# Kernel tuning notes

Measured on AMD Instinct MI355X. Metric: run time of the kernel, lower is better.

## Reference

```python
import jax, jax.numpy as jnp
import numpy as np

EPS = 1e-6

def _conv1x1(x, w, b):
    # x: [b,c,h,w], w: [o,c], b: [o] -> per-pixel matmul
    return jnp.einsum('bchw,oc->bohw', x, w) + b[None, :, None, None]

def setup_inputs() -> dict:
    key = jax.random.key(0)
    ks = jax.random.split(key, 10)
    b, c, h, w = 16, 256, 128, 128
    dec = jax.random.normal(ks[0], (b, c, h, w), jnp.float32)
    enc = jax.random.normal(ks[1], (b, c, h, w), jnp.float32)
    ln_w = jnp.ones((c,), jnp.float32)
    ln_b = jnp.zeros((c,), jnp.float32)
    w0 = jax.random.normal(ks[2], (c, c), jnp.float32) * 0.05
    b0 = jax.random.normal(ks[3], (c,), jnp.float32) * 0.05
    w1 = jax.random.normal(ks[4], (c // 2, c), jnp.float32) * 0.05
    b1 = jax.random.normal(ks[5], (c // 2,), jnp.float32) * 0.05
    w2 = jax.random.normal(ks[6], (c // 4, c // 2), jnp.float32) * 0.05
    b2 = jax.random.normal(ks[7], (c // 4,), jnp.float32) * 0.05
    w3 = jax.random.normal(ks[8], (1, c // 4), jnp.float32) * 0.05
    b3 = jax.random.normal(ks[9], (1,), jnp.float32) * 0.05
    return dict(dec=dec, enc=enc, ln_w=ln_w, ln_b=ln_b, w0=w0, b0=b0,
                w1=w1, b1=b1, w2=w2, b2=b2, w3=w3, b3=b3)

def reference(dec, enc, ln_w, ln_b, w0, b0, w1, b1, w2, b2, w3, b3):
    b, c, h, w = dec.shape
    x = dec + enc
    # LayerNorm2d: normalize over channel dim per pixel (biased var, eps=1e-6)
    mu = jnp.mean(x, axis=1, keepdims=True)
    var = jnp.var(x, axis=1, keepdims=True)
    x = (x - mu) / jnp.sqrt(var + EPS) * ln_w[None, :, None, None] + ln_b[None, :, None, None]
    # in_conv: 1x1 conv + exact GELU
    x = jax.nn.gelu(_conv1x1(x, w0, b0), approximate=False)
    # split: local channels kept, global channels pooled and broadcast back
    local_x = x[:, :c // 2]                                   # [b,c/2,h,w]
    global_x = jnp.mean(x[:, c // 2:], axis=(2, 3), keepdims=True)  # [b,c/2,1,1]
    x = jnp.concatenate([local_x, jnp.broadcast_to(global_x, local_x.shape)], axis=1)
    # mask_pre: nc -> nc/2 -> nc/4 -> 1 with GELUs
    x = jax.nn.gelu(_conv1x1(x, w1, b1), approximate=False)
    x = jax.nn.gelu(_conv1x1(x, w2, b2), approximate=False)
    x = _conv1x1(x, w3, b3)
    return jax.nn.sigmoid(x)
```

## Files before the change

kernel.cpp:

```cpp
#include <hip/hip_runtime.h>
#include <math.h>

typedef float f32x4 __attribute__((ext_vector_type(4)));
typedef short s8v __attribute__((ext_vector_type(8)));
typedef unsigned int u32x4 __attribute__((ext_vector_type(4)));

#define LN_EPS 1e-6f

static __device__ __forceinline__ unsigned short f2bf(float f) {
  union { float f; unsigned int u; } v; v.f = f;
  unsigned int r = (v.u + 0x7FFFu + ((v.u >> 16) & 1u)) >> 16;
  return (unsigned short)r;
}
static __device__ __forceinline__ float bf2f(unsigned short b) {
  union { float f; unsigned int u; } v; v.u = ((unsigned int)b) << 16;
  return v.f;
}
static __device__ __forceinline__ unsigned int f2bf_pk(float lo, float hi) {
  unsigned int r;
  asm("v_cvt_pk_bf16_f32 %0, %1, %2" : "=v"(r) : "v"(lo), "v"(hi));
  return r;
}
static __device__ __forceinline__ float gelu_fast(float x) {
  float t = x * x;
  float u = x * fmaf(t, 0.07135481283f, 1.5957691216f);
  float e = __expf(-u);
  return __fdividef(x, 1.0f + e);
}

__global__ void prep_kernel(const float* __restrict__ w0, const float* __restrict__ w1,
                            const float* __restrict__ w2, const float* __restrict__ lnw,
                            const float* __restrict__ lnb, const float* __restrict__ b0,
                            unsigned short* __restrict__ wt0f, unsigned short* __restrict__ w1f,
                            unsigned short* __restrict__ w2f, float* __restrict__ gacc,
                            float* __restrict__ sfold, float* __restrict__ tfold) {
  int idx = blockIdx.x * blockDim.x + threadIdx.x;
  int stride = gridDim.x * blockDim.x;
  const int N0 = 65536, N1 = 16384, N2 = 8192, N3 = 2048, N4 = 256;
  for (int i = idx; i < N0 + N1 + N2 + N3 + N4; i += stride) {
    if (i < N0) {
      int j = i & 7, l = (i >> 3) & 63, ks = (i >> 9) & 7, n0 = i >> 12;
      int k = ks * 32 + (l >> 4) * 8 + j;
      wt0f[i] = f2bf(w0[(n0 * 16 + (l & 15)) * 256 + k] * lnw[k]);
    } else if (i < N0 + N1) {
      int t = i - N0;
      int j = t & 7, l = (t >> 3) & 63, ks = (t >> 9) & 3, n0 = t >> 11;
      w1f[t] = f2bf(w1[(n0 * 16 + (l & 15)) * 256 + ks * 32 + (l >> 4) * 8 + j]);
    } else if (i < N0 + N1 + N2) {
      int t = i - N0 - N1;
      int j = t & 7, l = (t >> 3) & 63, ks = (t >> 9) & 3, n0 = t >> 11;
      w2f[t] = f2bf(w2[(n0 * 16 + (l & 15)) * 128 + ks * 32 + (l >> 4) * 8 + j]);
    } else if (i < N0 + N1 + N2 + N3) {
      gacc[i - N0 - N1 - N2] = 0.0f;
    } else {
      int n = i - N0 - N1 - N2 - N3;
      float s = 0.f, t = 0.f;
      for (int c = 0; c < 256; ++c) {
        float wv = w0[n * 256 + c];
        s += wv * lnw[c];
        t += wv * lnb[c];
      }
      sfold[n] = s;
      tfold[n] = t + b0[n];
    }
  }
}

__global__ __launch_bounds__(256, 4) void k1_kernel(
    const float* __restrict__ dec, const float* __restrict__ enc,
    const unsigned short* __restrict__ wt0f,
    const float* __restrict__ sfold, const float* __restrict__ tfold,
    unsigned short* __restrict__ yl, float* __restrict__ gacc) {
  __shared__ __align__(16) unsigned char At[64 * 512];
  __shared__ float wred[4][16][8];
  __shared__ float alphaL[64], betaL[64];

  const int tid = threadIdx.x, blk = blockIdx.x;
  const int b = blk >> 8;
  const int hw0 = (blk & 255) << 6;
  const int g = tid >> 4, kq = tid & 15;
  const int lane = tid & 63, w = tid >> 6, l15 = lane & 15, lg = lane >> 4;

  f32x4 sum = {0.f, 0.f, 0.f, 0.f}, sq = {0.f, 0.f, 0.f, 0.f};
  const long base = (long)(b * 256) * 16384 + hw0 + (kq << 2);
#pragma unroll
  for (int it = 0; it < 2; ++it) {
    f32x4 xv[8];
#pragma unroll
    for (int s = 0; s < 8; ++s) {
      const int c = it * 128 + g * 8 + s;
      f32x4 d = *(const f32x4*)(dec + base + (long)c * 16384);
      f32x4 e = *(const f32x4*)(enc + base + (long)c * 16384);
      f32x4 x = d + e;
      xv[s] = x;
      sum += x;
      sq += x * x;
    }
#pragma unroll
    for (int px = 0; px < 4; ++px) {
      const int p = (kq << 2) + px;
      u32x4 hv;
#pragma unroll
      for (int sp = 0; sp < 4; ++sp)
        hv[sp] = f2bf_pk(xv[2 * sp][px], xv[2 * sp + 1][px]);
      const int byte = (p * 512 + it * 256 + g * 16) ^ ((p & 7) << 4);
      *(u32x4*)(&At[byte]) = hv;
    }
  }

#pragma unroll
  for (int q = 0; q < 4; ++q) {
    sum[q] += __shfl_xor(sum[q], 16, 64);
    sq[q] += __shfl_xor(sq[q], 16, 64);
    sum[q] += __shfl_xor(sum[q], 32, 64);
    sq[q] += __shfl_xor(sq[q], 32, 64);
  }
  if (lane < 16) {
#pragma unroll
    for (int q = 0; q < 4; ++q) { wred[w][lane][q] = sum[q]; wred[w][lane][4 + q] = sq[q]; }
  }
  __syncthreads();
  if (tid < 64) {
    const int kk = tid >> 2, comp = tid & 3;
    float s = 0.f, s2 = 0.f;
#pragma unroll
    for (int ww = 0; ww < 4; ++ww) { s += wred[ww][kk][comp]; s2 += wred[ww][kk][4 + comp]; }
    const float mu = s * (1.0f / 256.0f);
    const float var = s2 * (1.0f / 256.0f) - mu * mu;
    const float rs = rsqrtf(var + LN_EPS);
    alphaL[tid] = rs;
    betaL[tid] = -mu * rs;
  }
  __syncthreads();

  f32x4 acc[4][4];
#pragma unroll
  for (int mi = 0; mi < 4; ++mi)
#pragma unroll
    for (int ni = 0; ni < 4; ++ni) acc[mi][ni] = (f32x4){0.f, 0.f, 0.f, 0.f};

#pragma unroll
  for (int ks = 0; ks < 8; ++ks) {
    s8v a[4];
#pragma unroll
    for (int mi = 0; mi < 4; ++mi) {
      const int p = mi * 16 + l15;
      const int byte = (p * 512 + ks * 64 + lg * 16) ^ ((p & 7) << 4);
      a[mi] = *(const s8v*)(&At[byte]);
    }
#pragma unroll
    for (int ni = 0; ni < 4; ++ni) {
      const int n0 = w * 4 + ni;
      s8v bfr = *(const s8v*)(wt0f + ((n0 * 8 + ks) * 64 + lane) * 8);
#pragma unroll
      for (int mi = 0; mi < 4; ++mi)
        acc[mi][ni] = __builtin_amdgcn_mfma_f32_16x16x32_bf16(a[mi], bfr, acc[mi][ni], 0, 0, 0);
    }
  }

  __syncthreads();

  float sn[4], tn[4];
#pragma unroll
  for (int ni = 0; ni < 4; ++ni) {
    const int n = w * 64 + ni * 16 + l15;
    sn[ni] = sfold[n];
    tn[ni] = tfold[n];
  }

  if (w < 2) {
#pragma unroll
    for (int mi = 0; mi < 4; ++mi) {
      const f32x4 al = *(const f32x4*)(&alphaL[mi * 16 + lg * 4]);
      const f32x4 be = *(const f32x4*)(&betaL[mi * 16 + lg * 4]);
#pragma unroll
      for (int r = 0; r < 4; ++r) {
        const int p = mi * 16 + lg * 4 + r;
#pragma unroll
        for (int ni = 0; ni < 4; ++ni) {
          const float v = gelu_fast(fmaf(al[r], acc[mi][ni][r], fmaf(be[r], sn[ni], tn[ni])));
          const int col = w * 64 + ni * 16 + l15;
          const int byte = (p * 256 + col * 2) ^ ((p & 7) << 4);
          *(unsigned short*)(&At[byte]) = f2bf(v);
        }
      }
    }
  } else {
    float ps[4] = {0.f, 0.f, 0.f, 0.f};
#pragma unroll
    for (int mi = 0; mi < 4; ++mi) {
      const f32x4 al = *(const f32x4*)(&alphaL[mi * 16 + lg * 4]);
      const f32x4 be = *(const f32x4*)(&betaL[mi * 16 + lg * 4]);
#pragma unroll
      for (int r = 0; r < 4; ++r) {
#pragma unroll
        for (int ni = 0; ni < 4; ++ni)
          ps[ni] += gelu_fast(fmaf(al[r], acc[mi][ni][r], fmaf(be[r], sn[ni], tn[ni])));
      }
    }
#pragma unroll
    for (int ni = 0; ni < 4; ++ni) {
      float p2 = ps[ni];
      p2 += __shfl_xor(p2, 16, 64);
      p2 += __shfl_xor(p2, 32, 64);
      if (lane < 16) atomicAdd(&gacc[b * 128 + (w - 2) * 64 + ni * 16 + lane], p2);
    }
  }
  __syncthreads();

  {
    const long rowbase = ((long)b * 16384 + hw0);
#pragma unroll
    for (int q = 0; q < 4; ++q) {
      const int p = q * 16 + (tid >> 4);
      const int colb = (tid & 15) * 16;
      const int byte = (p * 256 + colb) ^ ((p & 7) << 4);
      s8v v = *(const s8v*)(&At[byte]);
      __builtin_nontemporal_store(v, (s8v*)((char*)yl + (rowbase + p) * 256 + colb));
    }
  }
}

__global__ void kmid_kernel(const float* __restrict__ w1, const float* __restrict__ b1,
                            const float* __restrict__ gacc, float* __restrict__ g1) {
  int b = blockIdx.x, o = threadIdx.x;
  float acc = b1[o];
  const float inv = 1.0f / 16384.0f;
  for (int c = 0; c < 128; ++c)
    acc += w1[o * 256 + 128 + c] * (gacc[b * 128 + c] * inv);
  g1[b * 128 + o] = acc;
}

__global__ __launch_bounds__(256, 4) void k2_kernel(
    const unsigned short* __restrict__ yl, const float* __restrict__ g1,
    const float* __restrict__ b2v, const float* __restrict__ w3,
    const float* __restrict__ b3, const unsigned short* __restrict__ w1f,
    const unsigned short* __restrict__ w2f, float* __restrict__ out) {
  __shared__ __align__(16) unsigned char Yt[64 * 256];
  __shared__ __align__(16) unsigned char Z1[64 * 256];
  __shared__ __align__(16) unsigned char Z2[64 * 128];
  __shared__ float part3[4][64];
  __shared__ float w3S[64];

  const int tid = threadIdx.x, blk = blockIdx.x;
  const int lane = tid & 63, w = tid >> 6, l15 = lane & 15, lg = lane >> 4;
  const int P0 = blk * 64;
  const int b = blk >> 8;

  if (tid < 64) w3S[tid] = w3[tid];

#pragma unroll
  for (int q = 0; q < 4; ++q) {
    int p = q * 16 + (tid >> 4);
    int c2 = (tid & 15) * 16;
    s8v v = *(const s8v*)((const char*)yl + (long)(P0 + p) * 256 + c2);
    int byte = (p * 256 + c2) ^ ((p & 7) << 4);
    *(s8v*)(&Yt[byte]) = v;
  }
  __syncthreads();

  f32x4 acc1[4][2];
#pragma unroll
  for (int mi = 0; mi < 4; ++mi)
#pragma unroll
    for (int ni = 0; ni < 2; ++ni) acc1[mi][ni] = (f32x4){0.f, 0.f, 0.f, 0.f};
#pragma unroll
  for (int ks = 0; ks < 4; ++ks) {
    s8v a[4];
#pragma unroll
    for (int mi = 0; mi < 4; ++mi) {
      int p = mi * 16 + l15;
      int byte = (p * 256 + ks * 64 + lg * 16) ^ ((p & 7) << 4);
      a[mi] = *(const s8v*)(&Yt[byte]);
    }
#pragma unroll
    for (int ni = 0; ni < 2; ++ni) {
      int n0 = w * 2 + ni;
      s8v bfr = *(const s8v*)(w1f + ((n0 * 4 + ks) * 64 + lane) * 8);
#pragma unroll
      for (int mi = 0; mi < 4; ++mi)
        acc1[mi][ni] = __builtin_amdgcn_mfma_f32_16x16x32_bf16(a[mi], bfr, acc1[mi][ni], 0, 0, 0);
    }
  }
#pragma unroll
  for (int ni = 0; ni < 2; ++ni) {
    int o = (w * 2 + ni) * 16 + l15;
    float bias = g1[b * 128 + o];
#pragma unroll
    for (int mi = 0; mi < 4; ++mi)
#pragma unroll
      for (int r = 0; r < 4; ++r) {
        int p = mi * 16 + lg * 4 + r;
        float v = gelu_fast(acc1[mi][ni][r] + bias);
        int byte = (p * 256 + o * 2) ^ ((p & 7) << 4);
        *(unsigned short*)(&Z1[byte]) = f2bf(v);
      }
  }
  __syncthreads();

  f32x4 acc2[4];
#pragma unroll
  for (int mi = 0; mi < 4; ++mi) acc2[mi] = (f32x4){0.f, 0.f, 0.f, 0.f};
#pragma unroll
  for (int ks = 0; ks < 4; ++ks) {
    s8v a[4];
#pragma unroll
    for (int mi = 0; mi < 4; ++mi) {
      int p = mi * 16 + l15;
      int byte = (p * 256 + ks * 64 + lg * 16) ^ ((p & 7) << 4);
      a[mi] = *(const s8v*)(&Z1[byte]);
    }
    s8v bfr = *(const s8v*)(w2f + ((w * 4 + ks) * 64 + lane) * 8);
#pragma unroll
    for (int mi = 0; mi < 4; ++mi)
      acc2[mi] = __builtin_amdgcn_mfma_f32_16x16x32_bf16(a[mi], bfr, acc2[mi], 0, 0, 0);
  }
  {
    int o = w * 16 + l15;
    float bias = b2v[o];
#pragma unroll
    for (int mi = 0; mi < 4; ++mi)
#pragma unroll
      for (int r = 0; r < 4; ++r) {
        int p = mi * 16 + lg * 4 + r;
        float v = gelu_fast(acc2[mi][r] + bias);
        int byte = (p * 128 + o * 2) ^ ((p & 7) << 4);
        *(unsigned short*)(&Z2[byte]) = f2bf(v);
      }
  }
  __syncthreads();

  {
    int p = tid & 63, cg = tid >> 6;
    float dot = 0.f;
#pragma unroll
    for (int half = 0; half < 2; ++half) {
      int byte = (p * 128 + cg * 32 + half * 16) ^ ((p & 7) << 4);
      s8v z = *(const s8v*)(&Z2[byte]);
#pragma unroll
      for (int j = 0; j < 8; ++j)
        dot += bf2f((unsigned short)z[j]) * w3S[cg * 16 + half * 8 + j];
    }
    part3[cg][p] = dot;
  }
  __syncthreads();
  if (tid < 64) {
    float t = part3[0][tid] + part3[1][tid] + part3[2][tid] + part3[3][tid] + b3[0];
    out[P0 + tid] = __fdividef(1.0f, 1.0f + __expf(-t));
  }
}

extern "C" void kernel_launch(void* const* d_in, const int* in_sizes, int n_in,
                              void* d_out, int out_size, void* d_ws, size_t ws_size,
                              hipStream_t stream) {
  const float* dec = (const float*)d_in[0];
  const float* enc = (const float*)d_in[1];
  const float* lnw = (const float*)d_in[2];
  const float* lnb = (const float*)d_in[3];
  const float* w0  = (const float*)d_in[4];
  const float* b0  = (const float*)d_in[5];
  const float* w1  = (const float*)d_in[6];
  const float* b1  = (const float*)d_in[7];
  const float* w2  = (const float*)d_in[8];
  const float* b2  = (const float*)d_in[9];
  const float* w3  = (const float*)d_in[10];
  const float* b3  = (const float*)d_in[11];

  char* ws = (char*)d_ws;
  unsigned short* yl   = (unsigned short*)ws;
  unsigned short* wt0f = (unsigned short*)(ws + 67108864);
  unsigned short* w1f  = (unsigned short*)(ws + 67239936);
  unsigned short* w2f  = (unsigned short*)(ws + 67272704);
  float* gacc          = (float*)(ws + 67289088);
  float* g1            = (float*)(ws + 67297280);
  float* sfold         = (float*)(ws + 67305472);
  float* tfold         = (float*)(ws + 67306496);

  prep_kernel<<<128, 256, 0, stream>>>(w0, w1, w2, lnw, lnb, b0, wt0f, w1f, w2f,
                                       gacc, sfold, tfold);
  k1_kernel<<<4096, 256, 0, stream>>>(dec, enc, wt0f, sfold, tfold, yl, gacc);
  kmid_kernel<<<16, 128, 0, stream>>>(w1, b1, gacc, g1);
  k2_kernel<<<4096, 256, 0, stream>>>(yl, g1, b2, w3, b3, w1f, w2f, (float*)d_out);
}
```

Baseline: 215.0 us.

## Pipeline input loads with MFMA GEMM over channel quarters in k1

Splits k1's load, convert and GEMM phases into four channel quarters. Global loads for upcoming quarters are issued while the current quarter is converted to bf16 in LDS and fed to MFMA, so memory latency overlaps matrix compute. The LayerNorm statistics are reduced while the last quarter's GEMM runs. This needs two sets of prefetch registers, so the launch bound drops from 4 to 3 blocks per SM, trading occupancy for explicit software pipelining.

```diff
diff --git a/kernel.cpp b/kernel.cpp
--- a/kernel.cpp
+++ b/kernel.cpp
@@ -3,7 +3,6 @@
 
 typedef float f32x4 __attribute__((ext_vector_type(4)));
 typedef short s8v __attribute__((ext_vector_type(8)));
-typedef unsigned int u32x4 __attribute__((ext_vector_type(4)));
 
 #define LN_EPS 1e-6f
 
@@ -66,7 +65,53 @@
   }
 }
 
-__global__ __launch_bounds__(256, 4) void k1_kernel(
+
+#define ISSUE_Q(dr, er, q)                                                   \
+  _Pragma("unroll") for (int s = 0; s < 4; ++s) {                            \
+    const int c = (q) * 64 + g4 * 4 + s;                                     \
+    dr[s] = *(const f32x4*)(dec + base + (long)c * 16384);                   \
+    er[s] = *(const f32x4*)(enc + base + (long)c * 16384);                   \
+  }
+
+#define CONVERT_Q(dr, er, q) {                                               \
+  f32x4 xv[4];                                                               \
+  _Pragma("unroll") for (int s = 0; s < 4; ++s) {                            \
+    xv[s] = dr[s] + er[s]; sum += xv[s]; sq += xv[s] * xv[s];                \
+  }                                                                          \
+  _Pragma("unroll") for (int px = 0; px < 4; ++px) {                         \
+    const int p = (kq << 2) + px;                                            \
+    uint2 hv;                                                                \
+    hv.x = f2bf_pk(xv[0][px], xv[1][px]);                                    \
+    hv.y = f2bf_pk(xv[2][px], xv[3][px]);                                    \
+    const int byte = (p * 512 + (q) * 128 + g4 * 8) ^ ((p & 7) << 4);        \
+    *(uint2*)(&At[byte]) = hv;                                               \
+  } }
+
+#define GEMM_Q(q)                                                            \
+  _Pragma("unroll") for (int kk = 0; kk < 2; ++kk) {                         \
+    const int ks = (q) * 2 + kk;                                             \
+    s8v a[4];                                                                \
+    _Pragma("unroll") for (int mi = 0; mi < 4; ++mi) {                       \
+      const int p = mi * 16 + l15;                                           \
+      const int byte = (p * 512 + ks * 64 + lg * 16) ^ ((p & 7) << 4);       \
+      a[mi] = *(const s8v*)(&At[byte]);                                      \
+    }                                                                        \
+    _Pragma("unroll") for (int ni = 0; ni < 4; ++ni) {                       \
+      const int n0 = w * 4 + ni;                                             \
+      s8v bfr = *(const s8v*)(wt0f + ((n0 * 8 + ks) * 64 + lane) * 8);       \
+      _Pragma("unroll") for (int mi = 0; mi < 4; ++mi)                       \
+        acc[mi][ni] =                                                        \
+            __builtin_amdgcn_mfma_f32_16x16x32_bf16(a[mi], bfr, acc[mi][ni], 0, 0, 0); \
+    }                                                                        \
+  }
+
+#define LBAR() {                                                             \
+  asm volatile("s_waitcnt lgkmcnt(0)" ::: "memory");                         \
+  __builtin_amdgcn_s_barrier();                                              \
+  __builtin_amdgcn_sched_barrier(0);                                         \
+}
+
+__global__ __launch_bounds__(256, 3) void k1_kernel(
     const float* __restrict__ dec, const float* __restrict__ enc,
     const unsigned short* __restrict__ wt0f,
     const float* __restrict__ sfold, const float* __restrict__ tfold,
@@ -78,35 +123,38 @@
   const int tid = threadIdx.x, blk = blockIdx.x;
   const int b = blk >> 8;
   const int hw0 = (blk & 255) << 6;
-  const int g = tid >> 4, kq = tid & 15;
+  const int g4 = tid >> 4, kq = tid & 15;
   const int lane = tid & 63, w = tid >> 6, l15 = lane & 15, lg = lane >> 4;
 
+  const long base = (long)(b * 256) * 16384 + hw0 + (kq << 2);
+
   f32x4 sum = {0.f, 0.f, 0.f, 0.f}, sq = {0.f, 0.f, 0.f, 0.f};
-  const long base = (long)(b * 256) * 16384 + hw0 + (kq << 2);
-#pragma unroll
-  for (int it = 0; it < 2; ++it) {
-    f32x4 xv[8];
-#pragma unroll
-    for (int s = 0; s < 8; ++s) {
-      const int c = it * 128 + g * 8 + s;
-      f32x4 d = *(const f32x4*)(dec + base + (long)c * 16384);
-      f32x4 e = *(const f32x4*)(enc + base + (long)c * 16384);
-      f32x4 x = d + e;
-      xv[s] = x;
-      sum += x;
-      sq += x * x;
-    }
-#pragma unroll
-    for (int px = 0; px < 4; ++px) {
-      const int p = (kq << 2) + px;
-      u32x4 hv;
-#pragma unroll
-      for (int sp = 0; sp < 4; ++sp)
-        hv[sp] = f2bf_pk(xv[2 * sp][px], xv[2 * sp + 1][px]);
-      const int byte = (p * 512 + it * 256 + g * 16) ^ ((p & 7) << 4);
-      *(u32x4*)(&At[byte]) = hv;
-    }
-  }
+  f32x4 acc[4][4];
+#pragma unroll
+  for (int mi = 0; mi < 4; ++mi)
+#pragma unroll
+    for (int ni = 0; ni < 4; ++ni) acc[mi][ni] = (f32x4){0.f, 0.f, 0.f, 0.f};
+
+  f32x4 d0[4], e0[4], d1[4], e1[4];
+
+  ISSUE_Q(d0, e0, 0);
+  ISSUE_Q(d1, e1, 1);
+
+  CONVERT_Q(d0, e0, 0);
+  LBAR();
+  GEMM_Q(0);
+  ISSUE_Q(d0, e0, 2);
+
+  CONVERT_Q(d1, e1, 1);
+  LBAR();
+  GEMM_Q(1);
+  ISSUE_Q(d1, e1, 3);
+
+  CONVERT_Q(d0, e0, 2);
+  LBAR();
+  GEMM_Q(2);
+
+  CONVERT_Q(d1, e1, 3);
 
 #pragma unroll
   for (int q = 0; q < 4; ++q) {
@@ -120,6 +168,7 @@
     for (int q = 0; q < 4; ++q) { wred[w][lane][q] = sum[q]; wred[w][lane][4 + q] = sq[q]; }
   }
   __syncthreads();
+
   if (tid < 64) {
     const int kk = tid >> 2, comp = tid & 3;
     float s = 0.f, s2 = 0.f;
@@ -131,33 +180,7 @@
     alphaL[tid] = rs;
     betaL[tid] = -mu * rs;
   }
-  __syncthreads();
-
-  f32x4 acc[4][4];
-#pragma unroll
-  for (int mi = 0; mi < 4; ++mi)
-#pragma unroll
-    for (int ni = 0; ni < 4; ++ni) acc[mi][ni] = (f32x4){0.f, 0.f, 0.f, 0.f};
-
-#pragma unroll
-  for (int ks = 0; ks < 8; ++ks) {
-    s8v a[4];
-#pragma unroll
-    for (int mi = 0; mi < 4; ++mi) {
-      const int p = mi * 16 + l15;
-      const int byte = (p * 512 + ks * 64 + lg * 16) ^ ((p & 7) << 4);
-      a[mi] = *(const s8v*)(&At[byte]);
-    }
-#pragma unroll
-    for (int ni = 0; ni < 4; ++ni) {
-      const int n0 = w * 4 + ni;
-      s8v bfr = *(const s8v*)(wt0f + ((n0 * 8 + ks) * 64 + lane) * 8);
-#pragma unroll
-      for (int mi = 0; mi < 4; ++mi)
-        acc[mi][ni] = __builtin_amdgcn_mfma_f32_16x16x32_bf16(a[mi], bfr, acc[mi][ni], 0, 0, 0);
-    }
-  }
-
+  GEMM_Q(3);
   __syncthreads();
 
   float sn[4], tn[4];
```

After: 257.0 us. 1.2x slower.

## Stream dec/enc into LDS with async double-buffered global_load_lds in k1

Applied to the files above, without the earlier changes.

The LayerNorm/conv0 kernel now uses async global-to-LDS loads (global_load_lds) into a two-stage LDS buffer. Each wave loads its own 8-channel slab per stage and converts it to bf16 while the next stage is in flight, gated by explicit vmcnt waits. This replaces direct float4 register loads and lets loading overlap with conversion. The channel-stat reduction is simplified and one block barrier is removed. The extra 32KB of LDS lowers launch bounds from 4 to 2 blocks per CU, which cuts occupancy and may reduce memory-level parallelism in this bandwidth-bound stage.

```diff
diff --git a/kernel.cpp b/kernel.cpp
--- a/kernel.cpp
+++ b/kernel.cpp
@@ -26,6 +26,11 @@
   float u = x * fmaf(t, 0.07135481283f, 1.5957691216f);
   float e = __expf(-u);
   return __fdividef(x, 1.0f + e);
+}
+static __device__ __forceinline__ void gload16(const float* g, void* l) {
+  __builtin_amdgcn_global_load_lds(
+      (const __attribute__((address_space(1))) unsigned int*)(g),
+      (__attribute__((address_space(3))) unsigned int*)(l), 16, 0, 0);
 }
 
 __global__ void prep_kernel(const float* __restrict__ w0, const float* __restrict__ w1,
@@ -66,72 +71,79 @@
   }
 }
 
-__global__ __launch_bounds__(256, 4) void k1_kernel(
+
+#define ISSUE_E(e, buf) {                                                    \
+  _Pragma("unroll") for (int i = 0; i < 2; ++i) {                            \
+    const int row = (e) * 32 + w * 8 + i * 4 + (lane >> 4);                  \
+    const int col = (lane & 15) * 4;                                         \
+    gload16(decb + (long)row * 16384 + col, &DE[buf][w * 2048 + i * 1024]);  \
+    gload16(encb + (long)row * 16384 + col,                                  \
+            &DE[buf][8192 + w * 2048 + i * 1024]);                           \
+  } }
+
+#define CONV_E(e, buf) {                                                     \
+  const float* Dp = (const float*)&DE[buf][0];                               \
+  const float* Ep = (const float*)&DE[buf][8192];                            \
+  float xs[8];                                                               \
+  _Pragma("unroll") for (int j = 0; j < 8; ++j) {                            \
+    float d = Dp[(w * 8 + j) * 64 + lane];                                   \
+    float en = Ep[(w * 8 + j) * 64 + lane];                                  \
+    float x = d + en;                                                        \
+    sum1 += x; sq1 += x * x; xs[j] = x;                                      \
+  }                                                                          \
+  u32x4 hv;                                                                  \
+  _Pragma("unroll") for (int sp = 0; sp < 4; ++sp)                           \
+    hv[sp] = f2bf_pk(xs[2 * sp], xs[2 * sp + 1]);                            \
+  const int byte = (lane * 512 + ((e) * 32 + w * 8) * 2) ^ ((lane & 7) << 4);\
+  *(u32x4*)(&At[byte]) = hv;                                                 \
+}
+
+#define WAITV(n) { asm volatile("s_waitcnt vmcnt(" #n ")" ::: "memory");     \
+                   __builtin_amdgcn_sched_barrier(0); }
+
+__global__ __launch_bounds__(256, 2) void k1_kernel(
     const float* __restrict__ dec, const float* __restrict__ enc,
     const unsigned short* __restrict__ wt0f,
     const float* __restrict__ sfold, const float* __restrict__ tfold,
     unsigned short* __restrict__ yl, float* __restrict__ gacc) {
   __shared__ __align__(16) unsigned char At[64 * 512];
-  __shared__ float wred[4][16][8];
+  __shared__ __align__(16) unsigned char DE[2][16384];
+  __shared__ float wredS[4][64], wredQ[4][64];
   __shared__ float alphaL[64], betaL[64];
 
   const int tid = threadIdx.x, blk = blockIdx.x;
   const int b = blk >> 8;
   const int hw0 = (blk & 255) << 6;
-  const int g = tid >> 4, kq = tid & 15;
   const int lane = tid & 63, w = tid >> 6, l15 = lane & 15, lg = lane >> 4;
 
-  f32x4 sum = {0.f, 0.f, 0.f, 0.f}, sq = {0.f, 0.f, 0.f, 0.f};
-  const long base = (long)(b * 256) * 16384 + hw0 + (kq << 2);
-#pragma unroll
-  for (int it = 0; it < 2; ++it) {
-    f32x4 xv[8];
-#pragma unroll
-    for (int s = 0; s < 8; ++s) {
-      const int c = it * 128 + g * 8 + s;
-      f32x4 d = *(const f32x4*)(dec + base + (long)c * 16384);
-      f32x4 e = *(const f32x4*)(enc + base + (long)c * 16384);
-      f32x4 x = d + e;
-      xv[s] = x;
-      sum += x;
-      sq += x * x;
-    }
-#pragma unroll
-    for (int px = 0; px < 4; ++px) {
-      const int p = (kq << 2) + px;
-      u32x4 hv;
-#pragma unroll
-      for (int sp = 0; sp < 4; ++sp)
-        hv[sp] = f2bf_pk(xv[2 * sp][px], xv[2 * sp + 1][px]);
-      const int byte = (p * 512 + it * 256 + g * 16) ^ ((p & 7) << 4);
-      *(u32x4*)(&At[byte]) = hv;
-    }
-  }
-
-#pragma unroll
-  for (int q = 0; q < 4; ++q) {
-    sum[q] += __shfl_xor(sum[q], 16, 64);
-    sq[q] += __shfl_xor(sq[q], 16, 64);
-    sum[q] += __shfl_xor(sum[q], 32, 64);
-    sq[q] += __shfl_xor(sq[q], 32, 64);
-  }
-  if (lane < 16) {
-#pragma unroll
-    for (int q = 0; q < 4; ++q) { wred[w][lane][q] = sum[q]; wred[w][lane][4 + q] = sq[q]; }
-  }
-  __syncthreads();
+  const float* decb = dec + (long)b * 256 * 16384 + hw0;
+  const float* encb = enc + (long)b * 256 * 16384 + hw0;
+
+  float sum1 = 0.f, sq1 = 0.f;
+
+  ISSUE_E(0, 0); ISSUE_E(1, 1);
+  WAITV(4); CONV_E(0, 0); ISSUE_E(2, 0);
+  WAITV(4); CONV_E(1, 1); ISSUE_E(3, 1);
+  WAITV(4); CONV_E(2, 0); ISSUE_E(4, 0);
+  WAITV(4); CONV_E(3, 1); ISSUE_E(5, 1);
+  WAITV(4); CONV_E(4, 0); ISSUE_E(6, 0);
+  WAITV(4); CONV_E(5, 1); ISSUE_E(7, 1);
+  WAITV(4); CONV_E(6, 0);
+  WAITV(0); CONV_E(7, 1);
+
+  wredS[w][lane] = sum1;
+  wredQ[w][lane] = sq1;
+  __syncthreads();
+
   if (tid < 64) {
-    const int kk = tid >> 2, comp = tid & 3;
-    float s = 0.f, s2 = 0.f;
-#pragma unroll
-    for (int ww = 0; ww < 4; ++ww) { s += wred[ww][kk][comp]; s2 += wred[ww][kk][4 + comp]; }
+    float s = wredS[0][tid] + wredS[1][tid] + wredS[2][tid] + wredS[3][tid];
+    float s2 = wredQ[0][tid] + wredQ[1][tid] + wredQ[2][tid] + wredQ[3][tid];
     const float mu = s * (1.0f / 256.0f);
     const float var = s2 * (1.0f / 256.0f) - mu * mu;
     const float rs = rsqrtf(var + LN_EPS);
     alphaL[tid] = rs;
     betaL[tid] = -mu * rs;
   }
-  __syncthreads();
 
   f32x4 acc[4][4];
 #pragma unroll
@@ -157,7 +169,6 @@
         acc[mi][ni] = __builtin_amdgcn_mfma_f32_16x16x32_bf16(a[mi], bfr, acc[mi][ni], 0, 0, 0);
     }
   }
-
   __syncthreads();
 
   float sn[4], tn[4];
```

Measured after the change: 226.5 us. 1.05x slower.
